# Performance work log

Measured on AMD Instinct MI355X. Metric: run time of the kernel, lower is better.

The kernel has to match this reference:

```python
import jax, jax.numpy as jnp
import numpy as np
from jax import lax

V, H = 50257, 256
B, S, T = 128, 50, 32
TQ = 32


def position_encoding(emb):
    # emb: (B, S, T, H); l[s, e] = 1 - s/(T-1) - e/(H-1)*(1 - 2*s/(T-1))
    slen, elen = emb.shape[2], emb.shape[3]
    s = jnp.arange(slen, dtype=jnp.float32)[:, None] / (slen - 1)
    e = jnp.arange(elen, dtype=jnp.float32)[None, :] / (elen - 1)
    l = 1.0 - s - e * (1.0 - 2.0 * s)  # (T, H)
    return jnp.sum(emb * l[None, None], axis=2)  # (B, S, H)


def gru_seq(x, Wih, Whh, bih, bhh):
    # x: (B, T, H); torch GRU cell math; returns outputs (B,T,H), last hidden (B,H)
    h0 = jnp.zeros((x.shape[0], Whh.shape[1]), x.dtype)
    def step(h, xt):
        gi = xt @ Wih.T + bih
        gh = h @ Whh.T + bhh
        ir, iz, inn = jnp.split(gi, 3, axis=-1)
        hr, hz, hn = jnp.split(gh, 3, axis=-1)
        r = jax.nn.sigmoid(ir + hr)
        z = jax.nn.sigmoid(iz + hz)
        n = jnp.tanh(inn + r * hn)
        h_new = (1.0 - z) * n + z * h
        return h_new, h_new
    h_last, ys = lax.scan(step, h0, jnp.swapaxes(x, 0, 1))
    return jnp.swapaxes(ys, 0, 1), h_last


def setup_inputs() -> dict:
    key = jax.random.key(0)
    ks = jax.random.split(key, 16)
    def g(k, shape, scale=0.05):
        return (jax.random.normal(k, shape, dtype=jnp.float32) * scale)
    inp = {
        "contexts": jax.random.randint(ks[0], (B, S, T), 0, V, dtype=jnp.int32),
        "questions": jax.random.randint(ks[1], (B, TQ), 0, V, dtype=jnp.int32),
        "emb": jax.random.uniform(ks[2], (V, H), jnp.float32, -1.0, 1.0),
        "Wih_f": g(ks[3], (3 * H, H)), "Whh_f": g(ks[4], (3 * H, H)),
        "bih_f": jnp.zeros((3 * H,), jnp.float32), "bhh_f": jnp.zeros((3 * H,), jnp.float32),
        "Wih_b": g(ks[5], (3 * H, H)), "Whh_b": g(ks[6], (3 * H, H)),
        "bih_b": jnp.zeros((3 * H,), jnp.float32), "bhh_b": jnp.zeros((3 * H,), jnp.float32),
        "Wih_q": g(ks[7], (3 * H, H)), "Whh_q": g(ks[8], (3 * H, H)),
        "bih_q": jnp.zeros((3 * H,), jnp.float32), "bhh_q": jnp.zeros((3 * H,), jnp.float32),
        "Wo": g(ks[9], (V, H)), "bo": jnp.zeros((V,), jnp.float32),
    }
    return inp


def reference(contexts, questions, emb, Wih_f, Whh_f, bih_f, bhh_f,
              Wih_b, Whh_b, bih_b, bhh_b, Wih_q, Whh_q, bih_q, bhh_q, Wo, bo):
    # InputNet: embed -> position encoding -> bidirectional GRU (halves summed)
    ctx = emb[contexts]                      # (B, S, T, H)
    ctx = position_encoding(ctx)             # (B, S, H)  (dropout = eval no-op)
    out_f, _ = gru_seq(ctx, Wih_f, Whh_f, bih_f, bhh_f)
    out_b, _ = gru_seq(ctx[:, ::-1], Wih_b, Whh_b, bih_b, bhh_b)
    facts = out_f + out_b[:, ::-1]           # (B, S, H)
    # QuestionNet: embed -> GRU, take last hidden
    qemb = emb[questions]                    # (B, TQ, H)
    _, q = gru_seq(qemb, Wih_q, Whh_q, bih_q, bhh_q)   # (B, H)
    # AttnNet: dot-product scores + softmax over sentences (vectorized)
    energies = jnp.einsum('bsd,bd->bs', facts, q)
    attn = jax.nn.softmax(energies, axis=-1)           # (B, S)
    # memory read: bmm(attn, facts)
    read = jnp.einsum('bs,bsd->bd', attn, facts)       # (B, H)
    out = jnp.tanh(q * read) @ Wo.T + bo               # (B, V)
    return out
```

## Files before the change

### kernel.cpp

```cpp
#include <hip/hip_runtime.h>

#define V 50257
#define H 256
#define B 128
#define S 50
#define T 32
#define TQ 32

typedef __bf16 bf16x8 __attribute__((ext_vector_type(8)));
typedef float f32x4 __attribute__((ext_vector_type(4)));

__device__ inline unsigned short f2bf(float x) {
  __bf16 b = (__bf16)x;
  return __builtin_bit_cast(unsigned short, b);
}

__device__ inline float sigf(float x) {
  return 1.f / (1.f + __builtin_amdgcn_exp2f(-1.4426950408889634f * x));
}
__device__ inline float tanhfast(float x) {
  return 1.f - 2.f / (__builtin_amdgcn_exp2f(2.8853900817779268f * x) + 1.f);
}

__global__ __launch_bounds__(256) void k_wconv(
    const float* w0, const float* w1, const float* w2,
    const float* w3, const float* w4, const float* w5,
    unsigned short* dst) {
  int mat = blockIdx.x / 192;
  int blk = blockIdx.x % 192;
  const float* src = (mat == 0) ? w0 : (mat == 1) ? w1 : (mat == 2) ? w2
                   : (mat == 3) ? w3 : (mat == 4) ? w4 : w5;
  int off = blk * 1024 + threadIdx.x * 4;
  float4 v = *(const float4*)(src + off);
  unsigned short* d = dst + mat * 196608 + off;
  d[0] = f2bf(v.x); d[1] = f2bf(v.y); d[2] = f2bf(v.z); d[3] = f2bf(v.w);
}

__global__ __launch_bounds__(256) void k_embed(
    const int* __restrict__ ctx_idx, const int* __restrict__ q_idx,
    const float* __restrict__ emb,
    unsigned short* __restrict__ ctx_bf, unsigned short* __restrict__ q_bf) {
  int tid = threadIdx.x;
  int wv = tid >> 6, lane = tid & 63;
  int r = blockIdx.x * 4 + wv;
  if (r < B * S) {
    int myidx = ctx_idx[r * T + (lane & 31)];
    float e0 = (float)(lane * 4) * (1.f / 255.f);
    float4 acc = make_float4(0.f, 0.f, 0.f, 0.f);
    #pragma unroll 4
    for (int t = 0; t < T; ++t) {
      int id = __shfl(myidx, t, 64);
      float4 v = *(const float4*)&emb[(long)id * H + lane * 4];
      float tf = t * (1.f / 31.f);
      float a = 1.f - tf;
      float bb = 2.f * tf - 1.f;
      acc.x += (a + (e0 + 0.f * (1.f / 255.f)) * bb) * v.x;
      acc.y += (a + (e0 + 1.f * (1.f / 255.f)) * bb) * v.y;
      acc.z += (a + (e0 + 2.f * (1.f / 255.f)) * bb) * v.z;
      acc.w += (a + (e0 + 3.f * (1.f / 255.f)) * bb) * v.w;
    }
    ushort4 o;
    o.x = f2bf(acc.x); o.y = f2bf(acc.y); o.z = f2bf(acc.z); o.w = f2bf(acc.w);
    *(ushort4*)&ctx_bf[r * H + lane * 4] = o;
  } else {
    int rq = r - B * S;
    if (rq < B * TQ) {
      float4 v = *(const float4*)&emb[(long)q_idx[rq] * H + lane * 4];
      ushort4 o;
      o.x = f2bf(v.x); o.y = f2bf(v.y); o.z = f2bf(v.z); o.w = f2bf(v.w);
      *(ushort4*)&q_bf[rq * H + lane * 4] = o;
    }
  }
}

__global__ __launch_bounds__(256) void k_gemm(
    const unsigned short* __restrict__ Xb, const unsigned short* __restrict__ Wb,
    const float* __restrict__ bias, float* __restrict__ Out) {
  const int n0 = blockIdx.x * 64;
  const int m0 = blockIdx.y * 128;
  __shared__ unsigned short lA[128 * 40];
  __shared__ unsigned short lB[64 * 40];
  int tid = threadIdx.x;
  int lane = tid & 63, wv = tid >> 6;
  int lr = lane & 15, lg = lane >> 4;
  f32x4 acc[2][4] = {};
  int sr = tid >> 2, skk = (tid & 3) * 8;
  for (int kt = 0; kt < 8; ++kt) {
    int k0 = kt * 32;
    __syncthreads();
    *(uint4*)&lA[sr * 40 + skk]        = *(const uint4*)&Xb[(m0 + sr) * 256 + k0 + skk];
    *(uint4*)&lA[(sr + 64) * 40 + skk] = *(const uint4*)&Xb[(m0 + sr + 64) * 256 + k0 + skk];
    *(uint4*)&lB[sr * 40 + skk]        = *(const uint4*)&Wb[(n0 + sr) * 256 + k0 + skk];
    __syncthreads();
    bf16x8 av0 = *(const bf16x8*)&lA[(wv * 32 + lr) * 40 + lg * 8];
    bf16x8 av1 = *(const bf16x8*)&lA[(wv * 32 + 16 + lr) * 40 + lg * 8];
    #pragma unroll
    for (int nt = 0; nt < 4; ++nt) {
      bf16x8 bv = *(const bf16x8*)&lB[(nt * 16 + lr) * 40 + lg * 8];
      acc[0][nt] = __builtin_amdgcn_mfma_f32_16x16x32_bf16(av0, bv, acc[0][nt], 0, 0, 0);
      acc[1][nt] = __builtin_amdgcn_mfma_f32_16x16x32_bf16(av1, bv, acc[1][nt], 0, 0, 0);
    }
  }
  #pragma unroll
  for (int nt = 0; nt < 4; ++nt) {
    int col = n0 + nt * 16 + lr;
    float bs = bias[col];
    #pragma unroll
    for (int mt = 0; mt < 2; ++mt) {
      #pragma unroll
      for (int r = 0; r < 4; ++r) {
        int row = m0 + wv * 32 + mt * 16 + lg * 4 + r;
        Out[row * 768 + col] = acc[mt][nt][r] + bs;
      }
    }
  }
}

__global__ __launch_bounds__(512, 2) void k_rnn(
    const float* __restrict__ Gf, const float* __restrict__ Gb, const float* __restrict__ Gq,
    const unsigned short* __restrict__ WhF, const unsigned short* __restrict__ WhB,
    const unsigned short* __restrict__ WhQ,
    const float* __restrict__ bhF, const float* __restrict__ bhB, const float* __restrict__ bhQ,
    float* __restrict__ outF, float* __restrict__ outB, float* __restrict__ qvec) {
  int blk = blockIdx.x;
  int mode = blk >> 3;
  int rg = blk & 7;
  const float* G = (mode == 0) ? Gf : (mode == 1) ? Gb : Gq;
  const unsigned short* Wh = (mode == 0) ? WhF : (mode == 1) ? WhB : WhQ;
  const float* bh = (mode == 0) ? bhF : (mode == 1) ? bhB : bhQ;
  const int Tn = (mode == 2) ? TQ : S;
  const int SEQ = Tn;
  float* ob = (mode == 0) ? outF : outB;

  __shared__ unsigned short hb[16 * 264];

  int tid = threadIdx.x;
  int lane = tid & 63, wv = tid >> 6;
  int lr = lane & 15, lg = lane >> 4;

  for (int i = tid; i < 16 * 264; i += 512) hb[i] = 0;

  bf16x8 w[3][2][8];
  #pragma unroll
  for (int g = 0; g < 3; ++g)
    #pragma unroll
    for (int nt = 0; nt < 2; ++nt) {
      const unsigned short* wp = Wh + (g * 256 + wv * 32 + nt * 16 + lr) * 256 + lg * 8;
      #pragma unroll
      for (int kt = 0; kt < 8; ++kt)
        w[g][nt][kt] = *(const bf16x8*)(wp + kt * 32);
    }

  float bhv[3][2];
  #pragma unroll
  for (int g = 0; g < 3; ++g)
    #pragma unroll
    for (int nt = 0; nt < 2; ++nt)
      bhv[g][nt] = bh[g * 256 + wv * 32 + nt * 16 + lr];

  float hcur[2][4] = {};

  __syncthreads();

  for (int t = 0; t < Tn; ++t) {
    int s = (mode == 1) ? (S - 1 - t) : t;
    f32x4 acc[6] = {};
    #pragma unroll
    for (int kt = 0; kt < 8; ++kt) {
      bf16x8 a = *(const bf16x8*)&hb[lr * 264 + kt * 32 + lg * 8];
      #pragma unroll
      for (int g = 0; g < 3; ++g) {
        acc[g * 2 + 0] = __builtin_amdgcn_mfma_f32_16x16x32_bf16(a, w[g][0][kt], acc[g * 2 + 0], 0, 0, 0);
        acc[g * 2 + 1] = __builtin_amdgcn_mfma_f32_16x16x32_bf16(a, w[g][1][kt], acc[g * 2 + 1], 0, 0, 0);
      }
    }
    #pragma unroll
    for (int nt = 0; nt < 2; ++nt) {
      int j = wv * 32 + nt * 16 + lr;
      #pragma unroll
      for (int r = 0; r < 4; ++r) {
        int m = lg * 4 + r;
        long grow = (long)((rg * 16 + m) * SEQ + s) * 768;
        float xr = G[grow + j];
        float xz = G[grow + 256 + j];
        float xn = G[grow + 512 + j];
        float rr = sigf(xr + acc[0 + nt][r] + bhv[0][nt]);
        float zz = sigf(xz + acc[2 + nt][r] + bhv[1][nt]);
        float nn = tanhfast(xn + rr * (acc[4 + nt][r] + bhv[2][nt]));
        hcur[nt][r] = (1.f - zz) * nn + zz * hcur[nt][r];
      }
    }
    __syncthreads();
    #pragma unroll
    for (int nt = 0; nt < 2; ++nt) {
      int j = wv * 32 + nt * 16 + lr;
      #pragma unroll
      for (int r = 0; r < 4; ++r) {
        int m = lg * 4 + r;
        hb[m * 264 + j] = f2bf(hcur[nt][r]);
        if (mode != 2)
          ob[(long)((rg * 16 + m) * S + s) * H + j] = hcur[nt][r];
      }
    }
    __syncthreads();
  }

  if (mode == 2) {
    #pragma unroll
    for (int nt = 0; nt < 2; ++nt) {
      int j = wv * 32 + nt * 16 + lr;
      #pragma unroll
      for (int r = 0; r < 4; ++r) {
        int m = lg * 4 + r;
        qvec[(rg * 16 + m) * H + j] = hcur[nt][r];
      }
    }
  }
}

__global__ __launch_bounds__(256) void k_attn(
    const float* __restrict__ outF, const float* __restrict__ outB,
    const float* __restrict__ qvec, unsigned short* __restrict__ tqv) {
  int b = blockIdx.x, tid = threadIdx.x;
  __shared__ float fs[S * H];
  __shared__ float qs[H];
  __shared__ float es[S];
  qs[tid] = qvec[b * H + tid];
  for (int s = 0; s < S; ++s)
    fs[s * H + tid] = outF[(b * S + s) * H + tid] + outB[(b * S + s) * H + tid];
  __syncthreads();
  int lane = tid & 63, wv = tid >> 6;
  for (int s = wv; s < S; s += 4) {
    const float* fr = &fs[s * H];
    float p = 0.f;
    #pragma unroll
    for (int j = 0; j < 4; ++j) p += fr[lane * 4 + j] * qs[lane * 4 + j];
    #pragma unroll
    for (int off = 32; off > 0; off >>= 1) p += __shfl_xor(p, off, 64);
    if (lane == 0) es[s] = p;
  }
  __syncthreads();
  float mx = -1e30f;
  for (int s = 0; s < S; ++s) mx = fmaxf(mx, es[s]);
  float sum = 0.f;
  for (int s = 0; s < S; ++s) sum += expf(es[s] - mx);
  float inv = 1.f / sum;
  float rd = 0.f;
  for (int s = 0; s < S; ++s) rd += expf(es[s] - mx) * inv * fs[s * H + tid];
  tqv[b * H + tid] = f2bf(tanhf(qs[tid] * rd));
}

__global__ __launch_bounds__(256) void k_out(
    const unsigned short* __restrict__ tqv, const float* __restrict__ Wo,
    const float* __restrict__ bo, float* __restrict__ Out) {
  int n0 = blockIdx.x * 64;
  int tid = threadIdx.x, lane = tid & 63, wv = tid >> 6;
  int lr = lane & 15, lg = lane >> 4;
  __shared__ unsigned short lA[B * H];
  #pragma unroll
  for (int i = 0; i < 16; ++i) {
    int c = tid + i * 256;
    int row = c >> 5, kk = (c & 31) * 8;
    int dst = row * 512 + ((kk * 2) ^ ((row & 7) << 4));
    *(uint4*)((char*)lA + dst) = *(const uint4*)&tqv[row * H + kk];
  }
  __syncthreads();
  int vcol = n0 + wv * 16 + lr;
  int vc = (vcol < V) ? vcol : (V - 1);
  f32x4 acc[8] = {};
  for (int kt = 0; kt < 8; ++kt) {
    const float* wp = &Wo[vc * H + kt * 32 + lg * 8];
    float4 w0 = *(const float4*)wp;
    float4 w1 = *(const float4*)(wp + 4);
    bf16x8 bv;
    bv[0] = (__bf16)w0.x; bv[1] = (__bf16)w0.y; bv[2] = (__bf16)w0.z; bv[3] = (__bf16)w0.w;
    bv[4] = (__bf16)w1.x; bv[5] = (__bf16)w1.y; bv[6] = (__bf16)w1.z; bv[7] = (__bf16)w1.w;
    #pragma unroll
    for (int mt = 0; mt < 8; ++mt) {
      int row = mt * 16 + lr;
      int boff = row * 512 + ((kt * 64 + lg * 16) ^ ((row & 7) << 4));
      bf16x8 av = *(const bf16x8*)((const char*)lA + boff);
      acc[mt] = __builtin_amdgcn_mfma_f32_16x16x32_bf16(av, bv, acc[mt], 0, 0, 0);
    }
  }
  if (vcol < V) {
    float bs = bo[vcol];
    #pragma unroll
    for (int mt = 0; mt < 8; ++mt)
      #pragma unroll
      for (int r = 0; r < 4; ++r) {
        int row = mt * 16 + lg * 4 + r;
        Out[row * V + vcol] = acc[mt][r] + bs;
      }
  }
}

extern "C" void kernel_launch(void* const* d_in, const int* in_sizes, int n_in,
                              void* d_out, int out_size, void* d_ws, size_t ws_size,
                              hipStream_t stream) {
  const int* contexts  = (const int*)d_in[0];
  const int* questions = (const int*)d_in[1];
  const float* emb   = (const float*)d_in[2];
  const float* Wih_f = (const float*)d_in[3];
  const float* Whh_f = (const float*)d_in[4];
  const float* bih_f = (const float*)d_in[5];
  const float* bhh_f = (const float*)d_in[6];
  const float* Wih_b = (const float*)d_in[7];
  const float* Whh_b = (const float*)d_in[8];
  const float* bih_b = (const float*)d_in[9];
  const float* bhh_b = (const float*)d_in[10];
  const float* Wih_q = (const float*)d_in[11];
  const float* Whh_q = (const float*)d_in[12];
  const float* bih_q = (const float*)d_in[13];
  const float* bhh_q = (const float*)d_in[14];
  const float* Wo = (const float*)d_in[15];
  const float* bo = (const float*)d_in[16];
  float* out = (float*)d_out;

  char* ws = (char*)d_ws;
  unsigned short* ctx_bf = (unsigned short*)(ws);
  unsigned short* q_bf   = (unsigned short*)(ws + 3276800);
  unsigned short* wbf    = (unsigned short*)(ws + 5373952);
  unsigned short* WihF_b = wbf + 0 * 196608;
  unsigned short* WhhF_b = wbf + 1 * 196608;
  unsigned short* WihB_b = wbf + 2 * 196608;
  unsigned short* WhhB_b = wbf + 3 * 196608;
  unsigned short* WihQ_b = wbf + 4 * 196608;
  unsigned short* WhhQ_b = wbf + 5 * 196608;
  float* Gf   = (float*)(ws + 7733248);
  float* Gb   = (float*)(ws + 27394048);
  float* Gq   = (float*)(ws + 47054848);
  float* outFp = (float*)(ws + 59637760);
  float* outBp = (float*)(ws + 66191360);
  float* qvec = (float*)(ws + 72744960);
  unsigned short* tqv = (unsigned short*)(ws + 72876032);

  k_wconv<<<1152, 256, 0, stream>>>(Wih_f, Whh_f, Wih_b, Whh_b, Wih_q, Whh_q, wbf);
  k_embed<<<(B * S + B * TQ + 3) / 4, 256, 0, stream>>>(contexts, questions, emb, ctx_bf, q_bf);
  k_gemm<<<dim3(12, 50), 256, 0, stream>>>(ctx_bf, WihF_b, bih_f, Gf);
  k_gemm<<<dim3(12, 50), 256, 0, stream>>>(ctx_bf, WihB_b, bih_b, Gb);
  k_gemm<<<dim3(12, 32), 256, 0, stream>>>(q_bf, WihQ_b, bih_q, Gq);
  k_rnn<<<24, 512, 0, stream>>>(Gf, Gb, Gq, WhhF_b, WhhB_b, WhhQ_b,
                                bhh_f, bhh_b, bhh_q, outFp, outBp, qvec);
  k_attn<<<B, 256, 0, stream>>>(outFp, outBp, qvec, tqv);
  k_out<<<786, 256, 0, stream>>>(tqv, Wo, bo, out);
}
```

Measured before the change: 485.2 us.

## Store gate projections time-major and double-buffer the GRU hidden state

The input-projection GEMM now writes its output in (time, batch) order, and the recurrent kernel and attention read that layout. Each time step's gate loads then touch one contiguous slab instead of rows spaced a sequence apart. The recurrent kernel also ping-pongs the bf16 hidden state between two shared buffers, which removes one barrier per step. It pins the recurrent weights in registers through an empty asm constraint and a waves-per-EU attribute, which risks register pressure or spills.

```diff
diff --git a/kernel.cpp b/kernel.cpp
--- a/kernel.cpp
+++ b/kernel.cpp
@@ -75,7 +75,7 @@
 
 __global__ __launch_bounds__(256) void k_gemm(
     const unsigned short* __restrict__ Xb, const unsigned short* __restrict__ Wb,
-    const float* __restrict__ bias, float* __restrict__ Out) {
+    const float* __restrict__ bias, float* __restrict__ Out, int seq) {
   const int n0 = blockIdx.x * 64;
   const int m0 = blockIdx.y * 128;
   __shared__ unsigned short lA[128 * 40];
@@ -110,13 +110,17 @@
       #pragma unroll
       for (int r = 0; r < 4; ++r) {
         int row = m0 + wv * 32 + mt * 16 + lg * 4 + r;
-        Out[row * 768 + col] = acc[mt][nt][r] + bs;
-      }
-    }
-  }
-}
-
-__global__ __launch_bounds__(512, 2) void k_rnn(
+        int bidx = row / seq;
+        int ss = row - bidx * seq;
+        Out[(long)(ss * B + bidx) * 768 + col] = acc[mt][nt][r] + bs;
+      }
+    }
+  }
+}
+
+__global__ __launch_bounds__(512)
+__attribute__((amdgpu_waves_per_eu(2, 2)))
+void k_rnn(
     const float* __restrict__ Gf, const float* __restrict__ Gb, const float* __restrict__ Gq,
     const unsigned short* __restrict__ WhF, const unsigned short* __restrict__ WhB,
     const unsigned short* __restrict__ WhQ,
@@ -129,18 +133,17 @@
   const unsigned short* Wh = (mode == 0) ? WhF : (mode == 1) ? WhB : WhQ;
   const float* bh = (mode == 0) ? bhF : (mode == 1) ? bhB : bhQ;
   const int Tn = (mode == 2) ? TQ : S;
-  const int SEQ = Tn;
   float* ob = (mode == 0) ? outF : outB;
 
-  __shared__ unsigned short hb[16 * 264];
+  __shared__ unsigned short hb[2][16 * 264];
 
   int tid = threadIdx.x;
   int lane = tid & 63, wv = tid >> 6;
   int lr = lane & 15, lg = lane >> 4;
 
-  for (int i = tid; i < 16 * 264; i += 512) hb[i] = 0;
-
-  bf16x8 w[3][2][8];
+  for (int i = tid; i < 16 * 264; i += 512) { hb[0][i] = 0; hb[1][i] = 0; }
+
+  f32x4 w[48];
   #pragma unroll
   for (int g = 0; g < 3; ++g)
     #pragma unroll
@@ -148,8 +151,10 @@
       const unsigned short* wp = Wh + (g * 256 + wv * 32 + nt * 16 + lr) * 256 + lg * 8;
       #pragma unroll
       for (int kt = 0; kt < 8; ++kt)
-        w[g][nt][kt] = *(const bf16x8*)(wp + kt * 32);
-    }
+        w[g * 16 + nt * 8 + kt] = *(const f32x4*)(wp + kt * 32);
+    }
+  #pragma unroll
+  for (int i = 0; i < 48; ++i) asm volatile("" : "+v"(w[i]));
 
   float bhv[3][2];
   #pragma unroll
@@ -159,19 +164,22 @@
       bhv[g][nt] = bh[g * 256 + wv * 32 + nt * 16 + lr];
 
   float hcur[2][4] = {};
-
+  int cur = 0;
   __syncthreads();
 
   for (int t = 0; t < Tn; ++t) {
     int s = (mode == 1) ? (S - 1 - t) : t;
+    const float* Gs = G + (long)s * (128 * 768);
     f32x4 acc[6] = {};
     #pragma unroll
     for (int kt = 0; kt < 8; ++kt) {
-      bf16x8 a = *(const bf16x8*)&hb[lr * 264 + kt * 32 + lg * 8];
+      bf16x8 a = *(const bf16x8*)&hb[cur][lr * 264 + kt * 32 + lg * 8];
       #pragma unroll
       for (int g = 0; g < 3; ++g) {
-        acc[g * 2 + 0] = __builtin_amdgcn_mfma_f32_16x16x32_bf16(a, w[g][0][kt], acc[g * 2 + 0], 0, 0, 0);
-        acc[g * 2 + 1] = __builtin_amdgcn_mfma_f32_16x16x32_bf16(a, w[g][1][kt], acc[g * 2 + 1], 0, 0, 0);
+        acc[g * 2 + 0] = __builtin_amdgcn_mfma_f32_16x16x32_bf16(
+            a, __builtin_bit_cast(bf16x8, w[g * 16 + kt]), acc[g * 2 + 0], 0, 0, 0);
+        acc[g * 2 + 1] = __builtin_amdgcn_mfma_f32_16x16x32_bf16(
+            a, __builtin_bit_cast(bf16x8, w[g * 16 + 8 + kt]), acc[g * 2 + 1], 0, 0, 0);
       }
     }
     #pragma unroll
@@ -180,29 +188,29 @@
       #pragma unroll
       for (int r = 0; r < 4; ++r) {
         int m = lg * 4 + r;
-        long grow = (long)((rg * 16 + m) * SEQ + s) * 768;
-        float xr = G[grow + j];
-        float xz = G[grow + 256 + j];
-        float xn = G[grow + 512 + j];
+        long grow = (long)(rg * 16 + m) * 768;
+        float xr = Gs[grow + j];
+        float xz = Gs[grow + 256 + j];
+        float xn = Gs[grow + 512 + j];
         float rr = sigf(xr + acc[0 + nt][r] + bhv[0][nt]);
         float zz = sigf(xz + acc[2 + nt][r] + bhv[1][nt]);
         float nn = tanhfast(xn + rr * (acc[4 + nt][r] + bhv[2][nt]));
         hcur[nt][r] = (1.f - zz) * nn + zz * hcur[nt][r];
       }
     }
-    __syncthreads();
     #pragma unroll
     for (int nt = 0; nt < 2; ++nt) {
       int j = wv * 32 + nt * 16 + lr;
       #pragma unroll
       for (int r = 0; r < 4; ++r) {
         int m = lg * 4 + r;
-        hb[m * 264 + j] = f2bf(hcur[nt][r]);
+        hb[cur ^ 1][m * 264 + j] = f2bf(hcur[nt][r]);
         if (mode != 2)
-          ob[(long)((rg * 16 + m) * S + s) * H + j] = hcur[nt][r];
+          ob[(long)(s * B + rg * 16 + m) * H + j] = hcur[nt][r];
       }
     }
     __syncthreads();
+    cur ^= 1;
   }
 
   if (mode == 2) {
@@ -227,7 +235,7 @@
   __shared__ float es[S];
   qs[tid] = qvec[b * H + tid];
   for (int s = 0; s < S; ++s)
-    fs[s * H + tid] = outF[(b * S + s) * H + tid] + outB[(b * S + s) * H + tid];
+    fs[s * H + tid] = outF[(long)(s * B + b) * H + tid] + outB[(long)(s * B + b) * H + tid];
   __syncthreads();
   int lane = tid & 63, wv = tid >> 6;
   for (int s = wv; s < S; s += 4) {
@@ -337,9 +345,9 @@
 
   k_wconv<<<1152, 256, 0, stream>>>(Wih_f, Whh_f, Wih_b, Whh_b, Wih_q, Whh_q, wbf);
   k_embed<<<(B * S + B * TQ + 3) / 4, 256, 0, stream>>>(contexts, questions, emb, ctx_bf, q_bf);
-  k_gemm<<<dim3(12, 50), 256, 0, stream>>>(ctx_bf, WihF_b, bih_f, Gf);
-  k_gemm<<<dim3(12, 50), 256, 0, stream>>>(ctx_bf, WihB_b, bih_b, Gb);
-  k_gemm<<<dim3(12, 32), 256, 0, stream>>>(q_bf, WihQ_b, bih_q, Gq);
+  k_gemm<<<dim3(12, 50), 256, 0, stream>>>(ctx_bf, WihF_b, bih_f, Gf, S);
+  k_gemm<<<dim3(12, 50), 256, 0, stream>>>(ctx_bf, WihB_b, bih_b, Gb, S);
+  k_gemm<<<dim3(12, 32), 256, 0, stream>>>(q_bf, WihQ_b, bih_q, Gq, TQ);
   k_rnn<<<24, 512, 0, stream>>>(Gf, Gb, Gq, WhhF_b, WhhB_b, WhhQ_b,
                                 bhh_f, bhh_b, bhh_q, outFp, outBp, qvec);
   k_attn<<<B, 256, 0, stream>>>(outFp, outBp, qvec, tqv);
```

Result: faster. 426.2 us (-12.2%).
